# Optimization experiments

Hardware: AMD Instinct MI355X
Metric: run time of the kernel (lower is better)

The kernel has to match this reference:

```python
import jax, jax.numpy as jnp
import numpy as np

N = 512      # nodes
E = 512      # edges = nb-graph nodes
M = 16384    # nb-graph edges
FIN = 64     # in_node_nf
HID = 128    # hidden_nf
D = 32       # VTV_coord_nf (positional-encoding width)


def _silu(v):
    return v * jax.nn.sigmoid(v)


def _mlp(v, w1, b1, w2, b2):
    # 2-layer MLP with SiLU (matches MLP(in, out, [hidden]))
    return _silu(v @ w1 + b1) @ w2 + b2


def setup_inputs() -> dict:
    key = jax.random.key(0)
    ks = jax.random.split(key, 32)

    def lin(k, i, o, scale=None):
        s = (1.0 / np.sqrt(i)) if scale is None else scale
        return jax.random.normal(k, (i, o), dtype=jnp.float32) * jnp.float32(s)

    inp = {}
    inp['h'] = jax.random.normal(ks[0], (N, FIN), dtype=jnp.float32)
    inp['x'] = jax.random.normal(ks[1], (N, 3), dtype=jnp.float32)
    inp['edges'] = jax.random.randint(ks[2], (2, E), 0, N)
    inp['nb_edge'] = jax.random.randint(ks[3], (2, M), 0, E)
    inp['edge_attr'] = jax.random.normal(ks[4], (E, 4), dtype=jnp.float32)
    inp['nb_num_nodes'] = E  # python int (static)
    # edge_encoder: MLP(2*FIN -> HID -> FIN)
    inp['ew1'] = lin(ks[5], 2 * FIN, HID); inp['eb1'] = jnp.zeros((HID,), jnp.float32)
    inp['ew2'] = lin(ks[6], HID, FIN);     inp['eb2'] = jnp.zeros((FIN,), jnp.float32)
    # PPGN mlp1 / mlp2: MLP(D+FIN -> HID -> FIN)
    inp['p1w1'] = lin(ks[7], D + FIN, HID); inp['p1b1'] = jnp.zeros((HID,), jnp.float32)
    inp['p1w2'] = lin(ks[8], HID, FIN);     inp['p1b2'] = jnp.zeros((FIN,), jnp.float32)
    inp['p2w1'] = lin(ks[9], D + FIN, HID); inp['p2b1'] = jnp.zeros((HID,), jnp.float32)
    inp['p2w2'] = lin(ks[10], HID, FIN);    inp['p2b2'] = jnp.zeros((FIN,), jnp.float32)
    # PPGN output mlp: MLP(D+FIN+FIN -> HID -> FIN) on concat(skip, matmul)
    inp['p3w1'] = lin(ks[11], D + 2 * FIN, HID); inp['p3b1'] = jnp.zeros((HID,), jnp.float32)
    inp['p3w2'] = lin(ks[12], HID, FIN);         inp['p3b2'] = jnp.zeros((FIN,), jnp.float32)
    # IGN 2->1: linear over 5 basis ops
    inp['ign_w'] = lin(ks[13], 5 * FIN, FIN); inp['ign_b'] = jnp.zeros((FIN,), jnp.float32)
    # coord_mlp: Linear(FIN,HID), SiLU, Linear(HID,1,bias=False) with tiny init
    inp['cw1'] = lin(ks[14], FIN, HID); inp['cb1'] = jnp.zeros((HID,), jnp.float32)
    inp['cw2'] = lin(ks[15], HID, 1, scale=0.001)
    # node_dec: MLP(FIN -> HID -> FIN)
    inp['ndw1'] = lin(ks[16], FIN, HID); inp['ndb1'] = jnp.zeros((HID,), jnp.float32)
    inp['ndw2'] = lin(ks[17], HID, FIN); inp['ndb2'] = jnp.zeros((FIN,), jnp.float32)
    return inp


def reference(h, x, edges, nb_edge, edge_attr, nb_num_nodes,
              ew1, eb1, ew2, eb2,
              p1w1, p1b1, p1w2, p1b2,
              p2w1, p2b1, p2w2, p2b2,
              p3w1, p3b1, p3w2, p3b2,
              ign_w, ign_b,
              cw1, cb1, cw2,
              ndw1, ndb1, ndw2, ndb2):
    rows, cols = edges[0], edges[1]
    coord_diff = x[rows] - x[cols]                      # [E,3]
    nbr, nbc = nb_edge[0], nb_edge[1]
    # VTV: inner product of the two relative-position vectors of paired edges
    vtv = jnp.sum(coord_diff[nbr] * coord_diff[nbc], axis=-1)   # [M]
    # sinusoidal positional encoding, a_scale = D/2
    half = D // 2
    div_term = jnp.exp(jnp.log(jnp.float32(10000.0)) * (2.0 * jnp.arange(half, dtype=jnp.float32) / D))
    ang = vtv[:, None] * jnp.float32(D / 2) / div_term          # [M, D/2]
    pe = jnp.stack([jnp.sin(ang), jnp.cos(ang)], axis=-1).reshape(vtv.shape[0], D)
    # node-pair features per original edge
    efn = _mlp(jnp.concatenate([h[rows], h[cols]], axis=1), ew1, eb1, ew2, eb2)  # [E,FIN]
    nb_feat = jnp.concatenate([pe, efn[nbr] * efn[nbc]], axis=1)                 # [M, D+FIN]
    # densify nb-graph 2-tensor and run PPGN block
    En = nb_num_nodes
    T = jnp.zeros((En, En, nb_feat.shape[1]), dtype=nb_feat.dtype).at[nbr, nbc].add(nb_feat)
    m1 = _mlp(T, p1w1, p1b1, p1w2, p1b2)                 # [En,En,FIN]
    m2 = _mlp(T, p2w1, p2b1, p2w2, p2b2)
    mult = jnp.einsum('ikf,kjf->ijf', m1, m2)            # feature-wise matmul
    Tout = _mlp(jnp.concatenate([T, mult], axis=-1), p3w1, p3b1, p3w2, p3b2)
    # IGN 2->1: diag, row-sum, col-sum, total-sum, trace (broadcast)
    idx = jnp.arange(En)
    diag = Tout[idx, idx]                                # [En,FIN]
    rowsum = Tout.sum(axis=1)
    colsum = Tout.sum(axis=0)
    tot = jnp.broadcast_to(Tout.sum(axis=(0, 1)), diag.shape)
    tr = jnp.broadcast_to(diag.sum(axis=0), diag.shape)
    nb_t1 = jnp.concatenate([diag, rowsum, colsum, tot, tr], axis=1) @ ign_w + ign_b  # [En,FIN]
    # coord update: weighted coord_diff, segment-mean over source node
    w = _silu(nb_t1 @ cw1 + cb1) @ cw2                   # [E,1]
    trans = coord_diff * w
    Nn = x.shape[0]
    seg = jax.ops.segment_sum(trans, rows, num_segments=Nn)
    cnt = jax.ops.segment_sum(jnp.ones((rows.shape[0], 1), trans.dtype), rows, num_segments=Nn)
    x_new = x + seg / jnp.clip(cnt, 1.0)
    # node update: scatter_add edge features then residual MLP
    nb_t0 = jax.ops.segment_sum(nb_t1, rows, num_segments=Nn)
    h_new = h + _mlp(nb_t0, ndw1, ndb1, ndw2, ndb2)
    return (h_new, x_new, edge_attr)
```

## Files before the change

kernel.cpp:

```cpp
#include <hip/hip_runtime.h>
#include <hip/hip_bf16.h>

#define NN   512
#define EE   512
#define MM   16384

typedef float v4f __attribute__((ext_vector_type(4)));
typedef short short8v __attribute__((ext_vector_type(8)));

__device__ __forceinline__ float silu_f(float v) { return v / (1.0f + __expf(-v)); }
__device__ __forceinline__ float silu_fast(float v) {
  return v * __builtin_amdgcn_rcpf(1.0f + __expf(-v));
}

__global__ __launch_bounds__(128) void k_front(
    const float* __restrict__ h, const float* __restrict__ x,
    const int* __restrict__ edges, const int* __restrict__ nb_edge,
    const float* __restrict__ ew1, const float* __restrict__ eb1,
    const float* __restrict__ ew2, const float* __restrict__ eb2,
    const float* __restrict__ p1b1, const float* __restrict__ p1w2, const float* __restrict__ p1b2,
    const float* __restrict__ p2b1, const float* __restrict__ p2w2, const float* __restrict__ p2b2,
    const float* __restrict__ p3w1,
    float* __restrict__ coord_diff, float* __restrict__ efn,
    float* __restrict__ c1, float* __restrict__ c2,
    __hip_bfloat16* __restrict__ Wt, int* __restrict__ slotmap) {
  __shared__ float sm[256];
  int b = blockIdx.x, t = threadIdx.x;
  if (b < 512) {
    int r = edges[b], c = edges[EE + b];
    if (t < 3) coord_diff[b * 3 + t] = x[r * 3 + t] - x[c * 3 + t];
    if (t < 64) { sm[t] = h[r * 64 + t]; sm[64 + t] = h[c * 64 + t]; }
    __syncthreads();
    float acc = eb1[t];
    for (int k = 0; k < 128; ++k) acc += sm[k] * ew1[k * 128 + t];
    sm[128 + t] = silu_f(acc);
    __syncthreads();
    if (t < 64) {
      float o = eb2[t];
      for (int k = 0; k < 128; ++k) o += sm[128 + k] * ew2[k * 64 + t];
      efn[b * 64 + t] = o;
    }
  } else if (b == 512) {
    sm[t] = silu_f(p1b1[t]); sm[128 + t] = silu_f(p2b1[t]);
    __syncthreads();
    if (t < 64) {
      float a1 = p1b2[t], a2 = p2b2[t];
      for (int k = 0; k < 128; ++k) { a1 += sm[k] * p1w2[k * 64 + t]; a2 += sm[128 + k] * p2w2[k * 64 + t]; }
      c1[t] = a1; c2[t] = a2;
    }
  } else if (b < 577) {
    int e = (b - 513) * 128 + t;
    int hh = e >> 6, f = e & 63;
    Wt[hh * 64 + f] = __float2bfloat16(p3w1[(96 + f) * 128 + hh]);
  } else {
    int m = (b - 577) * 128 + t;
    int cell = nb_edge[m] * 512 + nb_edge[MM + m];
    atomicCAS(&slotmap[cell], -1, -2);
  }
}

__global__ __launch_bounds__(256) void k_compact(int* __restrict__ slotmap,
                                                 int* __restrict__ cells,
                                                 int* __restrict__ nC) {
  int cell = blockIdx.x * 256 + threadIdx.x;
  if (slotmap[cell] != -2) return;
  int s = atomicAdd(nC, 1);
  slotmap[cell] = s;
  cells[s] = cell;
}

__global__ __launch_bounds__(192) void k_scatterT(
    const int* __restrict__ nb_edge, const int* __restrict__ slotmap,
    const float* __restrict__ coord_diff, const float* __restrict__ efn,
    float* __restrict__ Tc) {
  int t = threadIdx.x;
  int sub = (t >= 96) ? 1 : 0;
  int c = t - sub * 96;
  int m = blockIdx.x * 2 + sub;
  int a = nb_edge[m], b = nb_edge[MM + m];
  int s = slotmap[a * 512 + b];
  float val;
  if (c < 32) {
    float vtv = coord_diff[a * 3 + 0] * coord_diff[b * 3 + 0]
              + coord_diff[a * 3 + 1] * coord_diff[b * 3 + 1]
              + coord_diff[a * 3 + 2] * coord_diff[b * 3 + 2];
    int i = c >> 1;
    float ang = vtv * 16.0f * __expf(-0.57564627324851143f * (float)i);
    val = (c & 1) ? cosf(ang) : sinf(ang);
  } else {
    int f = c - 32;
    val = efn[a * 64 + f] * efn[b * 64 + f];
  }
  atomicAdd(&Tc[s * 96 + c], val);
}

__global__ __launch_bounds__(128) void k_mlp96b(
    const int* __restrict__ cells, const int* __restrict__ nC, const float* __restrict__ Tc,
    const float* __restrict__ w11, const float* __restrict__ b11,
    const float* __restrict__ w12, const float* __restrict__ b12,
    const float* __restrict__ w21, const float* __restrict__ b21,
    const float* __restrict__ w22, const float* __restrict__ b22,
    const float* __restrict__ c1, const float* __restrict__ c2,
    const float* __restrict__ p3w1,
    __hip_bfloat16* __restrict__ D1d, __hip_bfloat16* __restrict__ D2dT,
    float* __restrict__ A, float* __restrict__ B,
    float* __restrict__ TWc) {
  __shared__ float xsT[96 * 8];
  __shared__ float hid[8][128];
  __shared__ int cl[8];
  int t = threadIdx.x;
  int nc = *nC;
  int s0 = blockIdx.x * 8;
  if (s0 >= nc) return;
  for (int e = t; e < 768; e += 128) xsT[(e % 96) * 8 + e / 96] = Tc[s0 * 96 + e];
  if (t < 8) cl[t] = (s0 + t < nc) ? cells[s0 + t] : 0;
  __syncthreads();
  float tw[8], a1[8], a2[8];
#pragma unroll
  for (int c = 0; c < 8; ++c) { tw[c] = 0.f; a1[c] = b11[t]; a2[c] = b21[t]; }
  for (int k = 0; k < 96; ++k) {
    float wt = p3w1[k * 128 + t];
    float w1v = w11[k * 128 + t];
    float w2v = w21[k * 128 + t];
    float4 xlo = *(const float4*)&xsT[k * 8];
    float4 xhi = *(const float4*)&xsT[k * 8 + 4];
    float xv[8] = {xlo.x, xlo.y, xlo.z, xlo.w, xhi.x, xhi.y, xhi.z, xhi.w};
#pragma unroll
    for (int c = 0; c < 8; ++c) {
      tw[c] += xv[c] * wt; a1[c] += xv[c] * w1v; a2[c] += xv[c] * w2v;
    }
  }
#pragma unroll
  for (int c = 0; c < 8; ++c) {
    if (s0 + c < nc) TWc[(s0 + c) * 128 + t] = tw[c];
    hid[c][t] = silu_f(a1[c]);
  }
  __syncthreads();
  {
    int hh = t & 63, cq = t >> 6;
    float o[4];
#pragma unroll
    for (int cc = 0; cc < 4; ++cc) o[cc] = b12[hh];
    for (int k = 0; k < 128; ++k) {
      float w = w12[k * 64 + hh];
#pragma unroll
      for (int cc = 0; cc < 4; ++cc) o[cc] += hid[cq * 4 + cc][k] * w;
    }
#pragma unroll
    for (int cc = 0; cc < 4; ++cc) {
      int c = cq * 4 + cc;
      if (s0 + c < nc) {
        float d = o[cc] - c1[hh];
        int cell = cl[c];
        int ai = cell >> 9, bj = cell & 511;
        atomicAdd(&A[ai * 64 + hh], d);
        D1d[(hh * 512 + ai) * 512 + bj] = __float2bfloat16(d);
      }
    }
  }
  __syncthreads();
#pragma unroll
  for (int c = 0; c < 8; ++c) hid[c][t] = silu_f(a2[c]);
  __syncthreads();
  {
    int hh = t & 63, cq = t >> 6;
    float o[4];
#pragma unroll
    for (int cc = 0; cc < 4; ++cc) o[cc] = b22[hh];
    for (int k = 0; k < 128; ++k) {
      float w = w22[k * 64 + hh];
#pragma unroll
      for (int cc = 0; cc < 4; ++cc) o[cc] += hid[cq * 4 + cc][k] * w;
    }
#pragma unroll
    for (int cc = 0; cc < 4; ++cc) {
      int c = cq * 4 + cc;
      if (s0 + c < nc) {
        float d = o[cc] - c2[hh];
        int cell = cl[c];
        int ai = cell >> 9, bj = cell & 511;
        atomicAdd(&B[bj * 64 + hh], d);
        D2dT[(hh * 512 + bj) * 512 + ai] = __float2bfloat16(d);
      }
    }
  }
}

__global__ __launch_bounds__(128) void k_uv(
    const float* __restrict__ A, const float* __restrict__ B,
    const float* __restrict__ c1, const float* __restrict__ c2,
    const float* __restrict__ p3w1, const float* __restrict__ p3b1,
    float* __restrict__ u, float* __restrict__ v) {
  __shared__ float vec[64];
  int i = blockIdx.x, y = blockIdx.y, t = threadIdx.x;
  if (t < 64)
    vec[t] = (y == 0) ? (512.0f * c1[t] * c2[t] + c2[t] * A[i * 64 + t])
                      : (c1[t] * B[i * 64 + t]);
  __syncthreads();
  float a = (y == 0) ? p3b1[t] : 0.f;
  for (int f = 0; f < 64; ++f) a += vec[f] * p3w1[(96 + f) * 128 + t];
  (y == 0 ? u : v)[i * 128 + t] = a;
}

__global__ __launch_bounds__(256) void k_einsum_mfma(
    const __hip_bfloat16* __restrict__ D1d,
    const __hip_bfloat16* __restrict__ D2dT,
    __hip_bfloat16* __restrict__ S_fij) {
  __shared__ short As[128 * 40];
  __shared__ short Bs[128 * 40];
  int b = blockIdx.x;
  int f = b >> 4;
  int i0 = ((b >> 2) & 3) * 128, j0 = (b & 3) * 128;
  int t = threadIdx.x;
  int w = t >> 6, lane = t & 63;
  int wy = w >> 1, wx = w & 1;
  int q = lane >> 4, l15 = lane & 15;
  const short* Ap = (const short*)D1d + f * 262144;
  const short* Bp = (const short*)D2dT + f * 262144;
  int row = t >> 1, seg = t & 1;
  v4f acc[4][4];
#pragma unroll
  for (int yi = 0; yi < 4; ++yi)
#pragma unroll
    for (int xj = 0; xj < 4; ++xj) acc[yi][xj] = (v4f){0.f, 0.f, 0.f, 0.f};
  for (int k0 = 0; k0 < 512; k0 += 32) {
    __syncthreads();
    const short8v* ga = (const short8v*)&Ap[(i0 + row) * 512 + k0 + seg * 16];
    const short8v* gb = (const short8v*)&Bp[(j0 + row) * 512 + k0 + seg * 16];
    *(short8v*)&As[row * 40 + seg * 16] = ga[0];
    *(short8v*)&As[row * 40 + seg * 16 + 8] = ga[1];
    *(short8v*)&Bs[row * 40 + seg * 16] = gb[0];
    *(short8v*)&Bs[row * 40 + seg * 16 + 8] = gb[1];
    __syncthreads();
    short8v af[4], bf[4];
#pragma unroll
    for (int x = 0; x < 4; ++x) {
      af[x] = *(const short8v*)&As[(wy * 64 + x * 16 + l15) * 40 + q * 8];
      bf[x] = *(const short8v*)&Bs[(wx * 64 + x * 16 + l15) * 40 + q * 8];
    }
#pragma unroll
    for (int yi = 0; yi < 4; ++yi)
#pragma unroll
      for (int xj = 0; xj < 4; ++xj)
        acc[yi][xj] = __builtin_amdgcn_mfma_f32_16x16x32_bf16(af[yi], bf[xj], acc[yi][xj], 0, 0, 0);
  }
#pragma unroll
  for (int yi = 0; yi < 4; ++yi)
#pragma unroll
    for (int r = 0; r < 4; ++r) {
      int irow = i0 + wy * 64 + yi * 16 + q * 4 + r;
#pragma unroll
      for (int xj = 0; xj < 4; ++xj)
        S_fij[(f * 512 + irow) * 512 + j0 + wx * 64 + xj * 16 + l15] =
            __float2bfloat16(acc[yi][xj][r]);
    }
}

__global__ __launch_bounds__(256) void k_transpose(
    const __hip_bfloat16* __restrict__ S_fij, __hip_bfloat16* __restrict__ S) {
  __shared__ short lds[64 * 72];
  int t = threadIdx.x;
  int ij0 = blockIdx.x * 64;
  const short* src = (const short*)S_fij;
#pragma unroll
  for (int p = 0; p < 2; ++p) {
    int f = p * 32 + (t >> 3), seg = t & 7;
    short8v ga = *(const short8v*)&src[f * 262144 + ij0 + seg * 8];
    int fgrp = f >> 3, flo = f & 7;
#pragma unroll
    for (int k = 0; k < 8; ++k) {
      int ij = seg * 8 + k;
      int swz = (fgrp ^ (ij & 7) ^ ((ij >> 3) & 7)) & 7;
      lds[ij * 72 + swz * 8 + flo] = ga[k];
    }
  }
  __syncthreads();
  short* dst = (short*)S;
#pragma unroll
  for (int p = 0; p < 2; ++p) {
    int ij = p * 32 + (t >> 3), fseg = t & 7;
    int swz = (fseg ^ (ij & 7) ^ ((ij >> 3) & 7)) & 7;
    short8v val = *(const short8v*)&lds[ij * 72 + swz * 8];
    *(short8v*)&dst[(ij0 + ij) * 64 + fseg * 8] = val;
  }
}

__global__ __launch_bounds__(256) void k_tout_mfma(
    const __hip_bfloat16* __restrict__ S, const float* __restrict__ u,
    const float* __restrict__ v, const __hip_bfloat16* __restrict__ Wt,
    float* __restrict__ row_part, float* __restrict__ col_part,
    float* __restrict__ diag_silu) {
  __shared__ __hip_bfloat16 WtL[128 * 72];
  __shared__ __hip_bfloat16 uvL[4096];
  __shared__ __hip_bfloat16 colbuf[4][16][140];
  int t = threadIdx.x;
  int w = t >> 6, lane = t & 63;
  int q = lane >> 4, l15 = lane & 15;
  int bi = blockIdx.x >> 5, bj = blockIdx.x & 31;
  int i0 = bi * 16, j0 = bj * 16;
  for (int e = t; e < 4096; e += 256) {
    int row = e >> 5, c2 = e & 31;
    ((unsigned*)WtL)[row * 36 + c2] = ((const unsigned*)Wt)[row * 32 + c2];
  }
  for (int e = t; e < 2048; e += 256)
    uvL[e] = __float2bfloat16(u[(i0 + (e >> 7)) * 128 + (e & 127)]);
  for (int e = t; e < 2048; e += 256)
    uvL[2048 + e] = __float2bfloat16(v[(j0 + (e >> 7)) * 128 + (e & 127)]);
  short8v a[4][2];
#pragma unroll
  for (int mt = 0; mt < 4; ++mt) {
    const short8v* sp =
        (const short8v*)&S[((i0 + w * 4 + mt) * 512 + j0 + l15) * 64];
    a[mt][0] = sp[q];
    a[mt][1] = sp[4 + q];
  }
  __syncthreads();
#pragma unroll
  for (int half = 0; half < 2; ++half) {
    v4f acc[4][4];
#pragma unroll
    for (int mt = 0; mt < 4; ++mt)
#pragma unroll
      for (int n4 = 0; n4 < 4; ++n4) {
        int nt = half * 4 + n4;
        const short8v* b0 = (const short8v*)&WtL[(nt * 16 + l15) * 72 + q * 8];
        const short8v* b1 = (const short8v*)&WtL[(nt * 16 + l15) * 72 + 32 + q * 8];
        v4f c = {0.f, 0.f, 0.f, 0.f};
        c = __builtin_amdgcn_mfma_f32_16x16x32_bf16(a[mt][0], *b0, c, 0, 0, 0);
        c = __builtin_amdgcn_mfma_f32_16x16x32_bf16(a[mt][1], *b1, c, 0, 0, 0);
        acc[mt][n4] = c;
      }
#pragma unroll
    for (int n4 = 0; n4 < 4; ++n4) {
      int nt = half * 4 + n4;
      int hh = nt * 16 + l15;
      float uu[4];
#pragma unroll
      for (int mt = 0; mt < 4; ++mt)
        uu[mt] = __bfloat162float(uvL[(w * 4 + mt) * 128 + hh]);
      float rs[4] = {0.f, 0.f, 0.f, 0.f};
#pragma unroll
      for (int r = 0; r < 4; ++r) {
        int jL = q * 4 + r;
        float cs = 0.f;
        float vv = __bfloat162float(uvL[2048 + jL * 128 + hh]);
#pragma unroll
        for (int mt = 0; mt < 4; ++mt) {
          int iL = w * 4 + mt;
          float sv = silu_fast(acc[mt][n4][r] + uu[mt] + vv);
          rs[mt] += sv;
          cs += sv;
          if (bi == bj && iL == jL) diag_silu[(i0 + iL) * 128 + hh] = sv;
        }
        colbuf[w][jL][hh] = __float2bfloat16(cs);
      }
#pragma unroll
      for (int mt = 0; mt < 4; ++mt) {
        float rsum = rs[mt];
        rsum += __shfl_xor(rsum, 16);
        rsum += __shfl_xor(rsum, 32);
        if (q == 0)
          row_part[(bj * 512 + i0 + w * 4 + mt) * 128 + hh] = rsum;
      }
    }
  }
  __syncthreads();
  for (int e = t; e < 2048; e += 256) {
    int jL = e >> 7, hh = e & 127;
    float acc4 = __bfloat162float(colbuf[0][jL][hh]) + __bfloat162float(colbuf[1][jL][hh]) +
                 __bfloat162float(colbuf[2][jL][hh]) + __bfloat162float(colbuf[3][jL][hh]);
    col_part[(bi * 512 + j0 + jL) * 128 + hh] = acc4;
  }
}

__global__ __launch_bounds__(128) void k_corr(
    const int* __restrict__ cells, const int* __restrict__ nC,
    const __hip_bfloat16* __restrict__ S, const float* __restrict__ u,
    const float* __restrict__ v, const float* __restrict__ TWc,
    const __hip_bfloat16* __restrict__ Wt,
    float* __restrict__ corr_row, float* __restrict__ corr_col,
    float* __restrict__ diag_silu) {
  __shared__ float sf[64];
  int s = blockIdx.x;
  if (s >= *nC) return;
  int t = threadIdx.x;
  int cell = cells[s];
  int ai = cell >> 9, bj = cell & 511;
  if (t < 64) sf[t] = __bfloat162float(S[(ai * 512 + bj) * 64 + t]);
  __syncthreads();
  float acc = 0.f;
  const __hip_bfloat16* wr = &Wt[t * 64];
  for (int f = 0; f < 64; ++f) acc += sf[f] * __bfloat162float(wr[f]);
  float z0 = acc + u[ai * 128 + t] + v[bj * 128 + t];
  float zc = z0 + TWc[s * 128 + t];
  float d = silu_fast(zc) - silu_fast(z0);
  atomicAdd(&corr_row[ai * 128 + t], d);
  atomicAdd(&corr_col[bj * 128 + t], d);
  if (ai == bj) atomicAdd(&diag_silu[ai * 128 + t], d);
}

__global__ __launch_bounds__(128) void k_tout2f(
    const float* __restrict__ diag_silu, const float* __restrict__ row_part,
    const float* __restrict__ col_part,
    const float* __restrict__ corr_row, const float* __restrict__ corr_col,
    const float* __restrict__ w2, const float* __restrict__ b2,
    float* __restrict__ diag_T, float* __restrict__ row_T, float* __restrict__ col_T,
    float* __restrict__ tot, float* __restrict__ tr) {
  __shared__ float in[128];
  int e = blockIdx.x, which = blockIdx.y, t = threadIdx.x;
  float a;
  if (which == 0) {
    a = diag_silu[e * 128 + t];
  } else {
    const float* src = (which == 1) ? row_part : col_part;
    a = (which == 1) ? corr_row[e * 128 + t] : corr_col[e * 128 + t];
    for (int p = 0; p < 32; ++p) a += src[(p * 512 + e) * 128 + t];
  }
  in[t] = a;
  __syncthreads();
  if (t < 64) {
    float o = 0.f;
    for (int k = 0; k < 128; ++k) o += in[k] * w2[k * 64 + t];
    float val = o + b2[t] * ((which == 0) ? 1.0f : 512.0f);
    if (which == 0)      { diag_T[e * 64 + t] = val; atomicAdd(&tr[t], val); }
    else if (which == 1) { row_T[e * 64 + t] = val; atomicAdd(&tot[t], val); }
    else                 { col_T[e * 64 + t] = val; }
  }
}

__global__ __launch_bounds__(64) void k_nbt1(
    const float* __restrict__ diag_T, const float* __restrict__ row_T,
    const float* __restrict__ col_T, const float* __restrict__ tot,
    const float* __restrict__ tr,
    const float* __restrict__ gw, const float* __restrict__ gb,
    float* __restrict__ nb_t1) {
  __shared__ float in[320];
  int e = blockIdx.x, t = threadIdx.x;
  in[t] = diag_T[e * 64 + t]; in[64 + t] = row_T[e * 64 + t];
  in[128 + t] = col_T[e * 64 + t]; in[192 + t] = tot[t]; in[256 + t] = tr[t];
  __syncthreads();
  float a = gb[t];
  for (int k = 0; k < 320; ++k) a += in[k] * gw[k * 64 + t];
  nb_t1[e * 64 + t] = a;
}

__global__ __launch_bounds__(128) void k_edge_out(
    const int* __restrict__ edges, const float* __restrict__ coord_diff,
    const float* __restrict__ nb_t1, const float* __restrict__ edge_attr,
    const float* __restrict__ cw1, const float* __restrict__ cb1,
    const float* __restrict__ cw2,
    float* __restrict__ seg, float* __restrict__ cnt, float* __restrict__ nb_t0,
    float* __restrict__ out_ea) {
  __shared__ float in[64];
  __shared__ float red[128];
  int e = blockIdx.x, t = threadIdx.x;
  if (t < 64) in[t] = nb_t1[e * 64 + t];
  __syncthreads();
  float a = cb1[t];
  for (int k = 0; k < 64; ++k) a += in[k] * cw1[k * 128 + t];
  red[t] = silu_f(a) * cw2[t];
  __syncthreads();
  for (int s2 = 64; s2 > 0; s2 >>= 1) {
    if (t < s2) red[t] += red[t + s2];
    __syncthreads();
  }
  float w = red[0];
  int r = edges[e];
  if (t < 3) atomicAdd(&seg[r * 3 + t], coord_diff[e * 3 + t] * w);
  if (t == 64) atomicAdd(&cnt[r], 1.0f);
  if (t < 64) atomicAdd(&nb_t0[r * 64 + t], in[t]);
  if (t < 4) out_ea[e * 4 + t] = edge_attr[e * 4 + t];
}

__global__ __launch_bounds__(128) void k_node_out(
    const float* __restrict__ h, const float* __restrict__ x,
    const float* __restrict__ seg, const float* __restrict__ cnt,
    const float* __restrict__ nb_t0,
    const float* __restrict__ w1, const float* __restrict__ b1,
    const float* __restrict__ w2, const float* __restrict__ b2,
    float* __restrict__ out_h, float* __restrict__ out_x) {
  __shared__ float in[64];
  __shared__ float hs[128];
  int n = blockIdx.x, t = threadIdx.x;
  if (t < 3) {
    float c = cnt[n]; if (c < 1.f) c = 1.f;
    out_x[n * 3 + t] = x[n * 3 + t] + seg[n * 3 + t] / c;
  }
  if (t < 64) in[t] = nb_t0[n * 64 + t];
  __syncthreads();
  float a = b1[t];
  for (int k = 0; k < 64; ++k) a += in[k] * w1[k * 128 + t];
  hs[t] = silu_f(a);
  __syncthreads();
  if (t < 64) {
    float o = b2[t];
    for (int k = 0; k < 128; ++k) o += hs[k] * w2[k * 64 + t];
    out_h[n * 64 + t] = h[n * 64 + t] + o;
  }
}

extern "C" void kernel_launch(void* const* d_in, const int* in_sizes, int n_in,
                              void* d_out, int out_size, void* d_ws, size_t ws_size,
                              hipStream_t stream) {
  (void)in_sizes; (void)n_in; (void)out_size; (void)ws_size;
  const float* h  = (const float*)d_in[0];
  const float* x  = (const float*)d_in[1];
  const int* edges   = (const int*)d_in[2];
  const int* nb_edge = (const int*)d_in[3];
  const float* edge_attr = (const float*)d_in[4];
  const float* ew1 = (const float*)d_in[6],  *eb1 = (const float*)d_in[7];
  const float* ew2 = (const float*)d_in[8],  *eb2 = (const float*)d_in[9];
  const float* p1w1 = (const float*)d_in[10], *p1b1 = (const float*)d_in[11];
  const float* p1w2 = (const float*)d_in[12], *p1b2 = (const float*)d_in[13];
  const float* p2w1 = (const float*)d_in[14], *p2b1 = (const float*)d_in[15];
  const float* p2w2 = (const float*)d_in[16], *p2b2 = (const float*)d_in[17];
  const float* p3w1 = (const float*)d_in[18], *p3b1 = (const float*)d_in[19];
  const float* p3w2 = (const float*)d_in[20], *p3b2 = (const float*)d_in[21];
  const float* ignw = (const float*)d_in[22], *ignb = (const float*)d_in[23];
  const float* cw1 = (const float*)d_in[24], *cb1 = (const float*)d_in[25];
  const float* cw2 = (const float*)d_in[26];
  const float* ndw1 = (const float*)d_in[27], *ndb1 = (const float*)d_in[28];
  const float* ndw2 = (const float*)d_in[29], *ndb2 = (const float*)d_in[30];

  char* ws = (char*)d_ws;
  __hip_bfloat16* D1d  = (__hip_bfloat16*)(ws + 0);
  __hip_bfloat16* S    = (__hip_bfloat16*)(ws + 0);
  __hip_bfloat16* D2dT = (__hip_bfloat16*)(ws + 33554432);
  __hip_bfloat16* S_fij = (__hip_bfloat16*)(ws + 67108864);
  float* row_part = (float*)(ws + 100663296);
  float* col_part = (float*)(ws + 117440512);
  float* Tc    = (float*)(ws + 134217728);
  int*   nC    = (int*)(ws + 140509184);
  float* A     = (float*)(ws + 140509200);
  float* B     = (float*)(ws + 140640272);
  float* seg   = (float*)(ws + 140771344);
  float* cnt   = (float*)(ws + 140777488);
  float* nb_t0 = (float*)(ws + 140779536);
  float* tot   = (float*)(ws + 140910608);
  float* tr    = (float*)(ws + 140910864);
  float* corr_row = (float*)(ws + 140911120);
  float* corr_col = (float*)(ws + 141173264);
  int*   slotmap  = (int*)(ws + 141435904);
  int*   cells    = (int*)(ws + 142484480);
  float* TWc      = (float*)(ws + 142550016);
  float* c1       = (float*)(ws + 150938624);
  float* c2       = (float*)(ws + 150938880);
  float* u        = (float*)(ws + 150939136);
  float* v        = (float*)(ws + 151201280);
  float* coord_diff  = (float*)(ws + 151463424);
  float* efn         = (float*)(ws + 151469568);
  float* diag_silu   = (float*)(ws + 151600640);
  float* diag_T      = (float*)(ws + 151862784);
  float* row_T       = (float*)(ws + 151993856);
  float* col_T       = (float*)(ws + 152124928);
  float* nb_t1       = (float*)(ws + 152256000);
  __hip_bfloat16* Wt  = (__hip_bfloat16*)(ws + 152387072);

  float* out_h  = (float*)d_out;
  float* out_x  = out_h + 512 * 64;
  float* out_ea = out_x + 512 * 3;

  hipMemsetAsync(ws, 0, 67108864, stream);
  hipMemsetAsync(slotmap, 0xFF, 1048576, stream);
  hipMemsetAsync(ws + 134217728, 0, 7217680, stream);

  k_front<<<705, 128, 0, stream>>>(h, x, edges, nb_edge,
                                   ew1, eb1, ew2, eb2,
                                   p1b1, p1w2, p1b2, p2b1, p2w2, p2b2, p3w1,
                                   coord_diff, efn, c1, c2, Wt, slotmap);
  k_compact<<<1024, 256, 0, stream>>>(slotmap, cells, nC);
  k_scatterT<<<8192, 192, 0, stream>>>(nb_edge, slotmap, coord_diff, efn, Tc);
  k_mlp96b<<<2048, 128, 0, stream>>>(cells, nC, Tc,
                                     p1w1, p1b1, p1w2, p1b2,
                                     p2w1, p2b1, p2w2, p2b2,
                                     c1, c2, p3w1, D1d, D2dT, A, B, TWc);
  k_uv<<<dim3(512, 2), 128, 0, stream>>>(A, B, c1, c2, p3w1, p3b1, u, v);
  k_einsum_mfma<<<1024, 256, 0, stream>>>(D1d, D2dT, S_fij);
  k_transpose<<<4096, 256, 0, stream>>>(S_fij, S);
  k_tout_mfma<<<1024, 256, 0, stream>>>(S, u, v, Wt,
                                        row_part, col_part, diag_silu);
  k_corr<<<16384, 128, 0, stream>>>(cells, nC, S, u, v, TWc, Wt,
                                    corr_row, corr_col, diag_silu);
  k_tout2f<<<dim3(512, 3), 128, 0, stream>>>(diag_silu, row_part, col_part,
                                             corr_row, corr_col,
                                             p3w2, p3b2, diag_T, row_T, col_T,
                                             tot, tr);
  k_nbt1<<<512, 64, 0, stream>>>(diag_T, row_T, col_T, tot, tr, ignw, ignb, nb_t1);
  k_edge_out<<<512, 128, 0, stream>>>(edges, coord_diff, nb_t1, edge_attr,
                                      cw1, cb1, cw2, seg, cnt, nb_t0, out_ea);
  k_node_out<<<512, 128, 0, stream>>>(h, x, seg, cnt, nb_t0,
                                      ndw1, ndb1, ndw2, ndb2, out_h, out_x);
}
```

Before: 401.0 us.

## Write compact D values then densify via slot maps instead of memset plus scatter

The MLP kernel now writes the per-cell D1/D2 values into compact slot-indexed buffers. A new densify kernel builds the dense bf16 D1d and D2dT tensors by looking up each cell in a slotmap or its transpose and writing zeros where no cell exists. This drops the 64 MB zero memset and the strided scattered bf16 stores, in exchange for an extra kernel that writes the full dense arrays coalesced and gathers from compact buffers. The slotmap memset doubles to also cover the transposed map.

```diff
diff --git a/kernel.cpp b/kernel.cpp
--- a/kernel.cpp
+++ b/kernel.cpp
@@ -60,12 +60,14 @@
 }
 
 __global__ __launch_bounds__(256) void k_compact(int* __restrict__ slotmap,
+                                                 int* __restrict__ slotmapT,
                                                  int* __restrict__ cells,
                                                  int* __restrict__ nC) {
   int cell = blockIdx.x * 256 + threadIdx.x;
   if (slotmap[cell] != -2) return;
   int s = atomicAdd(nC, 1);
   slotmap[cell] = s;
+  slotmapT[(cell & 511) * 512 + (cell >> 9)] = s;
   cells[s] = cell;
 }
 
@@ -102,7 +104,7 @@
     const float* __restrict__ w22, const float* __restrict__ b22,
     const float* __restrict__ c1, const float* __restrict__ c2,
     const float* __restrict__ p3w1,
-    __hip_bfloat16* __restrict__ D1d, __hip_bfloat16* __restrict__ D2dT,
+    __hip_bfloat16* __restrict__ Dc1, __hip_bfloat16* __restrict__ Dc2,
     float* __restrict__ A, float* __restrict__ B,
     float* __restrict__ TWc) {
   __shared__ float xsT[96 * 8];
@@ -152,9 +154,9 @@
       if (s0 + c < nc) {
         float d = o[cc] - c1[hh];
         int cell = cl[c];
-        int ai = cell >> 9, bj = cell & 511;
+        int ai = cell >> 9;
         atomicAdd(&A[ai * 64 + hh], d);
-        D1d[(hh * 512 + ai) * 512 + bj] = __float2bfloat16(d);
+        Dc1[(s0 + c) * 64 + hh] = __float2bfloat16(d);
       }
     }
   }
@@ -178,12 +180,33 @@
       if (s0 + c < nc) {
         float d = o[cc] - c2[hh];
         int cell = cl[c];
-        int ai = cell >> 9, bj = cell & 511;
+        int bj = cell & 511;
         atomicAdd(&B[bj * 64 + hh], d);
-        D2dT[(hh * 512 + bj) * 512 + ai] = __float2bfloat16(d);
+        Dc2[(s0 + c) * 64 + hh] = __float2bfloat16(d);
       }
     }
   }
+}
+
+__global__ __launch_bounds__(128) void k_densify(
+    const int* __restrict__ slotmap, const int* __restrict__ slotmapT,
+    const __hip_bfloat16* __restrict__ Dc1, const __hip_bfloat16* __restrict__ Dc2,
+    __hip_bfloat16* __restrict__ D1d, __hip_bfloat16* __restrict__ D2dT) {
+  int b = blockIdx.x;
+  int f = b >> 9, row = b & 511;
+  int t = threadIdx.x;
+  int which = blockIdx.y;
+  const int* sm = which ? &slotmapT[row * 512] : &slotmap[row * 512];
+  const unsigned short* Dc = (const unsigned short*)(which ? Dc2 : Dc1);
+  unsigned short* dst = (unsigned short*)(which ? &D2dT[(f * 512 + row) * 512]
+                                                : &D1d[(f * 512 + row) * 512]);
+  int4 s4 = *(const int4*)&sm[t * 4];
+  ushort4 o;
+  o.x = (s4.x >= 0) ? Dc[s4.x * 64 + f] : 0;
+  o.y = (s4.y >= 0) ? Dc[s4.y * 64 + f] : 0;
+  o.z = (s4.z >= 0) ? Dc[s4.z * 64 + f] : 0;
+  o.w = (s4.w >= 0) ? Dc[s4.w * 64 + f] : 0;
+  *(ushort4*)&dst[t * 4] = o;
 }
 
 __global__ __launch_bounds__(128) void k_uv(
@@ -541,39 +564,43 @@
   float* corr_row = (float*)(ws + 140911120);
   float* corr_col = (float*)(ws + 141173264);
   int*   slotmap  = (int*)(ws + 141435904);
-  int*   cells    = (int*)(ws + 142484480);
-  float* TWc      = (float*)(ws + 142550016);
-  float* c1       = (float*)(ws + 150938624);
-  float* c2       = (float*)(ws + 150938880);
-  float* u        = (float*)(ws + 150939136);
-  float* v        = (float*)(ws + 151201280);
-  float* coord_diff  = (float*)(ws + 151463424);
-  float* efn         = (float*)(ws + 151469568);
-  float* diag_silu   = (float*)(ws + 151600640);
-  float* diag_T      = (float*)(ws + 151862784);
-  float* row_T       = (float*)(ws + 151993856);
-  float* col_T       = (float*)(ws + 152124928);
-  float* nb_t1       = (float*)(ws + 152256000);
-  __hip_bfloat16* Wt  = (__hip_bfloat16*)(ws + 152387072);
+  int*   slotmapT = (int*)(ws + 142484480);
+  int*   cells    = (int*)(ws + 143533056);
+  __hip_bfloat16* Dc1 = (__hip_bfloat16*)(ws + 143598592);
+  __hip_bfloat16* Dc2 = (__hip_bfloat16*)(ws + 145695744);
+  float* TWc      = (float*)(ws + 147792896);
+  float* c1       = (float*)(ws + 156181504);
+  float* c2       = (float*)(ws + 156181760);
+  float* u        = (float*)(ws + 156182016);
+  float* v        = (float*)(ws + 156444160);
+  float* coord_diff  = (float*)(ws + 156706304);
+  float* efn         = (float*)(ws + 156712448);
+  float* diag_silu   = (float*)(ws + 156843520);
+  float* diag_T      = (float*)(ws + 157105664);
+  float* row_T       = (float*)(ws + 157236736);
+  float* col_T       = (float*)(ws + 157367808);
+  float* nb_t1       = (float*)(ws + 157498880);
+  __hip_bfloat16* Wt  = (__hip_bfloat16*)(ws + 157629952);
 
   float* out_h  = (float*)d_out;
   float* out_x  = out_h + 512 * 64;
   float* out_ea = out_x + 512 * 3;
 
-  hipMemsetAsync(ws, 0, 67108864, stream);
-  hipMemsetAsync(slotmap, 0xFF, 1048576, stream);
+  hipMemsetAsync(slotmap, 0xFF, 2097152, stream);
   hipMemsetAsync(ws + 134217728, 0, 7217680, stream);
 
   k_front<<<705, 128, 0, stream>>>(h, x, edges, nb_edge,
                                    ew1, eb1, ew2, eb2,
                                    p1b1, p1w2, p1b2, p2b1, p2w2, p2b2, p3w1,
                                    coord_diff, efn, c1, c2, Wt, slotmap);
-  k_compact<<<1024, 256, 0, stream>>>(slotmap, cells, nC);
+  k_compact<<<1024, 256, 0, stream>>>(slotmap, slotmapT, cells, nC);
   k_scatterT<<<8192, 192, 0, stream>>>(nb_edge, slotmap, coord_diff, efn, Tc);
   k_mlp96b<<<2048, 128, 0, stream>>>(cells, nC, Tc,
                                      p1w1, p1b1, p1w2, p1b2,
                                      p2w1, p2b1, p2w2, p2b2,
-                                     c1, c2, p3w1, D1d, D2dT, A, B, TWc);
+                                     c1, c2, p3w1, Dc1, Dc2, A, B, TWc);
+  k_densify<<<dim3(32768, 2), 128, 0, stream>>>(slotmap, slotmapT, Dc1, Dc2,
+                                                D1d, D2dT);
   k_uv<<<dim3(512, 2), 128, 0, stream>>>(A, B, c1, c2, p3w1, p3b1, u, v);
   k_einsum_mfma<<<1024, 256, 0, stream>>>(D1d, D2dT, S_fij);
   k_transpose<<<4096, 256, 0, stream>>>(S_fij, S);
```

Result: no change. 408.9 us (+2.0%).
